# Optimization experiments

Hardware: AMD Instinct MI355X
Metric: run time of the kernel (lower is better)

The kernel has to match this reference:

```python
import jax, jax.numpy as jnp
import numpy as np

M = 32  # m = nsample_q


def _shared_mlp(x, layers):
    # x: [B, C, S, K]; each layer is 1x1 conv (pointwise) + bias + ReLU
    for W, b in layers:
        x = jax.nn.relu(jnp.einsum('oc,bcsk->bosk', W, x) + b[None, :, None, None])
    return x


def _conv_params(key, c_in, c_out):
    k1, k2 = jax.random.split(key)
    scale = 1.0 / np.sqrt(c_in)
    W = jax.random.uniform(k1, (c_out, c_in), jnp.float32, -scale, scale)
    b = jax.random.uniform(k2, (c_out,), jnp.float32, -scale, scale)
    return W, b


def setup_inputs() -> dict:
    key = jax.random.key(0)
    ks = jax.random.split(key, 12)
    B, S, C = 2, 8192, 64
    inp = {
        'xyz1': jax.random.normal(ks[0], (B, 3, S), jnp.float32),
        'feature1': jax.random.normal(ks[1], (B, C, S), jnp.float32),
        'xyz2': jax.random.normal(ks[2], (B, 3, S), jnp.float32),
        'feature2': jax.random.normal(ks[3], (B, C, S), jnp.float32),
    }
    # mlp1_spec = [64+64+10, 64, 64]
    inp['w_mlp1_0'], inp['b_mlp1_0'] = _conv_params(ks[4], 138, 64)
    inp['w_mlp1_1'], inp['b_mlp1_1'] = _conv_params(ks[5], 64, 64)
    # xyz encoders: [10 -> 64]
    inp['w_xyz1'], inp['b_xyz1'] = _conv_params(ks[6], 10, 64)
    inp['w_xyz2'], inp['b_xyz2'] = _conv_params(ks[7], 10, 64)
    # mlp2_spec = [128, 64, 64]
    inp['w_mlp2_0'], inp['b_mlp2_0'] = _conv_params(ks[8], 128, 64)
    inp['w_mlp2_1'], inp['b_mlp2_1'] = _conv_params(ks[9], 64, 64)
    # mlp3_spec = [192, 64, 64]
    inp['w_mlp3_0'], inp['b_mlp3_0'] = _conv_params(ks[10], 192, 64)
    inp['w_mlp3_1'], inp['b_mlp3_1'] = _conv_params(ks[11], 64, 64)
    return inp


def _arc_indices(S, m):
    # stage-1: each point attends to all m points of its arc (static, numpy)
    base = (np.arange(S) // m) * m
    idx_q = base[:, None] + np.arange(m)[None, :]          # [S, m]
    # stage-2: the other m-1 points of the arc (excluding self)
    pos = np.arange(S) % m
    mask = np.arange(m)[None, :] != pos[:, None]
    idx_rem = idx_q[mask].reshape(S, m - 1)                 # [S, m-1]
    return jnp.asarray(idx_q), jnp.asarray(idx_rem)


def reference(xyz1, feature1, xyz2, feature2,
              w_mlp1_0, b_mlp1_0, w_mlp1_1, b_mlp1_1,
              w_xyz1, b_xyz1, w_xyz2, b_xyz2,
              w_mlp2_0, b_mlp2_0, w_mlp2_1, b_mlp2_1,
              w_mlp3_0, b_mlp3_0, w_mlp3_1, b_mlp3_1):
    B, _, S = xyz1.shape
    idx_q, idx_rem = _arc_indices(S, M)

    # ---- stage 1: cross-frame cost volume over arc neighbors in frame2 ----
    qi_xyz = xyz2[:, :, idx_q]                 # [B,3,S,M]
    qi_feat = feature2[:, :, idx_q]            # [B,C,S,M]
    pi_xyz = xyz1[:, :, :, None]               # [B,3,S,1] (broadcast as tile)
    pi_feat = feature1[:, :, :, None]
    d_xyz = qi_xyz - pi_xyz
    euc = jnp.sqrt(jnp.sum(d_xyz * d_xyz, axis=1, keepdims=True) + 1e-20)
    pi_xyz_cat = jnp.concatenate(
        [jnp.broadcast_to(pi_xyz, qi_xyz.shape), qi_xyz, d_xyz, euc], axis=1)  # [B,10,S,M]
    feat_cat = jnp.concatenate(
        [jnp.broadcast_to(pi_feat, qi_feat.shape), qi_feat], axis=1)           # [B,2C,S,M]
    x = jnp.concatenate([pi_xyz_cat, feat_cat], axis=1)                         # [B,10+2C,S,M]
    pi_new = _shared_mlp(x, [(w_mlp1_0, b_mlp1_0), (w_mlp1_1, b_mlp1_1)])       # [B,64,S,M]
    pi_enc = _shared_mlp(pi_xyz_cat, [(w_xyz1, b_xyz1)])                        # [B,64,S,M]
    pi_cat = _shared_mlp(jnp.concatenate([pi_enc, pi_new], axis=1),
                         [(w_mlp2_0, b_mlp2_0), (w_mlp2_1, b_mlp2_1)])          # [B,64,S,M]
    WQ = jax.nn.softmax(pi_cat, axis=3)
    pi_agg = jnp.sum(WQ * pi_new, axis=3)                                       # [B,64,S]

    # ---- stage 2: intra-frame smoothing over remaining arc points ----
    pc_xyz_g = xyz1[:, :, idx_rem]             # [B,3,S,M-1]
    pc_pts_g = pi_agg[:, :, idx_rem]           # [B,64,S,M-1]
    pc_xyz_n = xyz1[:, :, :, None]
    pc_pts_n = feature1[:, :, :, None]
    d2 = pc_xyz_g - pc_xyz_n
    euc2 = jnp.sqrt(jnp.sum(d2 * d2, axis=1, keepdims=True) + 1e-20)
    pc_xyz_cat = jnp.concatenate(
        [jnp.broadcast_to(pc_xyz_n, pc_xyz_g.shape), pc_xyz_g, d2, euc2], axis=1)  # [B,10,S,M-1]
    pc_enc = _shared_mlp(pc_xyz_cat, [(w_xyz2, b_xyz2)])                           # [B,64,S,M-1]
    pc_cat = jnp.concatenate(
        [pc_enc, jnp.broadcast_to(pc_pts_n, (pc_pts_n.shape[:3] + (M - 1,))), pc_pts_g],
        axis=1)                                                                    # [B,192,S,M-1]
    pc_cat = _shared_mlp(pc_cat, [(w_mlp3_0, b_mlp3_0), (w_mlp3_1, b_mlp3_1)])
    WP = jax.nn.softmax(pc_cat, axis=3)
    return jnp.sum(WP * pc_pts_g, axis=3)      # [B,64,S]
```

## Files before the change

kernel.cpp:

```cpp
#include <hip/hip_runtime.h>


typedef __attribute__((ext_vector_type(8))) short   short8;
typedef __attribute__((ext_vector_type(8))) __bf16  bf16x8;
typedef __attribute__((ext_vector_type(4))) float   f32x4;
typedef __attribute__((ext_vector_type(4))) float   float4v;
typedef __attribute__((ext_vector_type(2))) unsigned int uint2v;
typedef __attribute__((ext_vector_type(4))) unsigned int uint4v;

#define S_LEN 8192
#define TPB   256
#define LOG2E 1.4426950408889634f

#define WSO_L11   0
#define WSO_L20   8192
#define WSO_L21   24576
#define WSO_L30A  32768
#define WSO_L31   40960
#define WS_WF1    49152
#define WS_WF2    57344
#define WS_W30B   65536
#define WS_W30C   73728
#define WS_F32    81920

#define OFF_W     0
#define OFF_ACT   32768
#define OFF_A1B   65536
#define OFF_A2B   69632
#define OFF_AGGB  73728
#define OFF_X1    77824
#define OFF_X2    78336
#define LDS_TOTAL 78848

__device__ __forceinline__ unsigned short f2bf(float f){
  unsigned int u = __float_as_uint(f);
  u += 0x7fffu + ((u >> 16) & 1u);
  return (unsigned short)(u >> 16);
}
__device__ __forceinline__ float bf2f(unsigned short h){
  return __uint_as_float(((unsigned int)h) << 16);
}
__device__ __forceinline__ unsigned cvtpk(float lo, float hi){
  unsigned r;
  asm("v_cvt_pk_bf16_f32 %0, %1, %2" : "=v"(r) : "v"(lo), "v"(hi));
  return r;
}
__device__ __forceinline__ float exp2a(float x){
  float r; asm("v_exp_f32 %0, %1" : "=v"(r) : "v"(x)); return r;
}

__device__ __forceinline__ bf16x8 ldsA(const char* base, int r, int k){
  short8 a = *(const short8*)(base + ((((r << 6) + k) << 1) ^ ((r & 7) << 4)));
  return __builtin_bit_cast(bf16x8, a);
}
__device__ __forceinline__ void stBF(char* base, int r, int c, float v){
  *(unsigned short*)(base + ((((r << 6) + c) << 1) ^ ((r & 7) << 4))) = f2bf(v);
}
__device__ __forceinline__ float ldBF(const char* base, int r, int c){
  return bf2f(*(const unsigned short*)(base + ((((r << 6) + c) << 1) ^ ((r & 7) << 4))));
}
__device__ __forceinline__ void stBF4(char* base, int r, int c4, float4v v){
  uint2v u; u.x = cvtpk(v.x, v.y); u.y = cvtpk(v.z, v.w);
  *(uint2v*)(base + ((((r << 6) + c4) << 1) ^ ((r & 7) << 4))) = u;
}
__device__ __forceinline__ float4v ldBF4(const char* base, int r, int c4){
  uint2v u = *(const uint2v*)(base + ((((r << 6) + c4) << 1) ^ ((r & 7) << 4)));
  float4v f;
  f.x = bf2f((unsigned short)(u.x & 0xffffu));
  f.y = bf2f((unsigned short)(u.x >> 16));
  f.z = bf2f((unsigned short)(u.y & 0xffffu));
  f.w = bf2f((unsigned short)(u.y >> 16));
  return f;
}

__device__ __forceinline__ void gemm_k64(f32x4 acc[4], const char* Asrc,
                                         const char* Bp, int rbase, int lane){
  const int r  = rbase + (lane & 15);
  const int kg = (lane >> 4) << 3;
#pragma unroll
  for (int kb = 0; kb < 2; ++kb){
    bf16x8 a = ldsA(Asrc, r, kb * 32 + kg);
#pragma unroll
    for (int cb = 0; cb < 4; ++cb){
      short8 braw = *(const short8*)(Bp + (((kb << 2) + cb) * 64 + lane) * 16);
      acc[cb] = __builtin_amdgcn_mfma_f32_16x16x32_bf16(
          a, __builtin_bit_cast(bf16x8, braw), acc[cb], 0, 0, 0);
    }
  }
}

__device__ __forceinline__ void gemm32_k64B(f32x4 acc[2][4], const char* Asrc,
                                            const char* Bp, int lane){
  const int kg = (lane >> 4) << 3;
#pragma unroll
  for (int t = 0; t < 2; ++t){
    const int r = t * 16 + (lane & 15);
#pragma unroll
    for (int kb = 0; kb < 2; ++kb){
      bf16x8 a = ldsA(Asrc, r, kb * 32 + kg);
#pragma unroll
      for (int cb = 0; cb < 4; ++cb){
        short8 braw = *(const short8*)(Bp + (((kb << 2) + cb) * 64 + lane) * 16);
        acc[t][cb] = __builtin_amdgcn_mfma_f32_16x16x32_bf16(
            a, __builtin_bit_cast(bf16x8, braw), acc[t][cb], 0, 0, 0);
      }
    }
  }
}

__device__ __forceinline__ void gemm_chL(f32x4 acc[2][4], const char* act,
                                         const char* Wp, int l15, int kg, int lane){
#pragma unroll
  for (int kb = 0; kb < 2; ++kb){
    bf16x8 W[4];
#pragma unroll
    for (int mb = 0; mb < 4; ++mb)
      W[mb] = __builtin_bit_cast(bf16x8,
          *(const short8*)(Wp + (((kb << 2) + mb) * 64 + lane) * 16));
#pragma unroll
    for (int nb = 0; nb < 2; ++nb){
      bf16x8 bfrag = ldsA(act, nb * 16 + l15, kb * 32 + kg);
#pragma unroll
      for (int mb = 0; mb < 4; ++mb)
        acc[nb][mb] = __builtin_amdgcn_mfma_f32_16x16x32_bf16(
            W[mb], bfrag, acc[nb][mb], 0, 0, 0);
    }
  }
}

__device__ __forceinline__ void store_ch(char* dst, f32x4 acc[2][4],
                                         const float4v bias4[4], int l15, int g){
#pragma unroll
  for (int nb = 0; nb < 2; ++nb){
    const int row = nb * 16 + l15;
    const int rb  = row << 7;
    const int swz = (row & 7) << 4;
#pragma unroll
    for (int mb = 0; mb < 4; ++mb){
      f32x4 z = acc[nb][mb] + bias4[mb];
      z.x=fmaxf(z.x,0.f); z.y=fmaxf(z.y,0.f); z.z=fmaxf(z.z,0.f); z.w=fmaxf(z.w,0.f);
      uint2v u; u.x = cvtpk(z.x, z.y); u.y = cvtpk(z.z, z.w);
      *(uint2v*)(dst + (rb + ((mb * 32 + g * 8) ^ swz))) = u;
    }
  }
}

__device__ __forceinline__ float red_max(float x){
  x = fmaxf(x, __shfl_xor(x, 16, 64));
  x = fmaxf(x, __shfl_xor(x, 32, 64));
  return x;
}
__device__ __forceinline__ float red_sum(float x){
  x += __shfl_xor(x, 16, 64);
  x += __shfl_xor(x, 32, 64);
  return x;
}

__global__ void pack_weights(const float* __restrict__ w10, const float* __restrict__ w11,
                             const float* __restrict__ wx1, const float* __restrict__ wx2,
                             const float* __restrict__ w20, const float* __restrict__ w21,
                             const float* __restrict__ w30, const float* __restrict__ w31,
                             unsigned char* __restrict__ ws)
{
  for (int i = blockIdx.x * blockDim.x + threadIdx.x; i < 42304;
       i += gridDim.x * blockDim.x){
    if (i < 40960){
      const float* src; int stride, coff, e;
      if      (i <  4096){ src = w11; stride =  64; coff =   0; e = i;         }
      else if (i < 12288){ src = w20; stride = 128; coff =   0; e = i -  4096; }
      else if (i < 16384){ src = w21; stride =  64; coff =   0; e = i - 12288; }
      else if (i < 20480){ src = w30; stride = 192; coff =   0; e = i - 16384; }
      else if (i < 24576){ src = w31; stride =  64; coff =   0; e = i - 20480; }
      else if (i < 28672){ src = w10; stride = 138; coff =  10; e = i - 24576; }
      else if (i < 32768){ src = w10; stride = 138; coff =  74; e = i - 28672; }
      else if (i < 36864){ src = w30; stride = 192; coff =  64; e = i - 32768; }
      else               { src = w30; stride = 192; coff = 128; e = i - 36864; }
      int j = e & 7, lane = (e >> 3) & 63, cb = (e >> 9) & 3, kb = e >> 11;
      int k = kb * 32 + ((lane >> 4) << 3) + j;
      int o = cb * 16 + (lane & 15);
      float val = src[o * stride + coff + k];
      if ((i >= 12288 && i < 16384) || (i >= 20480 && i < 24576)) val *= LOG2E;
      ((unsigned short*)ws)[i] = f2bf(val);
    } else {
      int f = i - 40960; float v;
      if (f < 1152){
        int grp = f / 192, rem = f % 192, d = rem >> 6, o = rem & 63;
        if      (grp == 0) v = w10[o*138 + d]     - w10[o*138 + 6 + d];
        else if (grp == 1) v = w10[o*138 + 3 + d] + w10[o*138 + 6 + d];
        else if (grp == 2) v = wx1[o*10 + d]      - wx1[o*10 + 6 + d];
        else if (grp == 3) v = wx1[o*10 + 3 + d]  + wx1[o*10 + 6 + d];
        else if (grp == 4) v = wx2[o*10 + d]      - wx2[o*10 + 6 + d];
        else               v = wx2[o*10 + 3 + d]  + wx2[o*10 + 6 + d];
      }
      else if (f < 1216) v = w10[(f - 1152)*138 + 9];
      else if (f < 1280) v = wx1[(f - 1216)*10  + 9];
      else               v = wx2[(f - 1280)*10  + 9];
      ((float*)(ws + WS_F32))[f] = v;
    }
  }
}

__global__ __launch_bounds__(TPB, 2) void cvkernel(
    const float* __restrict__ xyz1, const float* __restrict__ feat1,
    const float* __restrict__ xyz2, const float* __restrict__ feat2,
    const float* __restrict__ b10v, const float* __restrict__ bx1v,
    const float* __restrict__ b11v, const float* __restrict__ b20v,
    const float* __restrict__ b21v, const float* __restrict__ bx2v,
    const float* __restrict__ b30v, const float* __restrict__ b31v,
    const char*  __restrict__ ws,   float* __restrict__ out)
{
  extern __shared__ __align__(16) char smem[];
  const int tid  = threadIdx.x;
  const int lane = tid & 63;
  const int wave = tid >> 6;
  const int l15  = lane & 15;
  const int lg   = lane >> 4;
  const int kg   = lg << 3;
  const int tile = blockIdx.x;
  const int b    = tile >> 8;
  const int s0   = (tile & 255) << 5;

  float* x1   = (float*)(smem + OFF_X1);
  float* x2   = (float*)(smem + OFF_X2);
  char*  a1B  = smem + OFF_A1B;
  char*  a2B  = smem + OFF_A2B;
  char*  aggB = smem + OFF_AGGB;
  char*  wlds = smem + OFF_W;
  const float* cw = (const float*)(ws + WS_F32);

  char* myA = smem + OFF_ACT + wave * 8192;
  char* myB = myA + 4096;

  { const uint4v* src = (const uint4v*)ws;
    uint4v*       dst = (uint4v*)wlds;
    for (int i = tid; i < 2048; i += TPB) dst[i] = src[i]; }
  if (tid < 32){
#pragma unroll
    for (int d = 0; d < 3; ++d) x1[tid*4+d] = xyz1[(b*3+d)*S_LEN + s0 + tid];
    x1[tid*4+3] = 0.f;
  } else if (tid < 64){
    int p = tid - 32;
#pragma unroll
    for (int d = 0; d < 3; ++d) x2[p*4+d] = xyz2[(b*3+d)*S_LEN + s0 + p];
    x2[p*4+3] = 0.f;
  }
  for (int i = tid; i < 2048; i += TPB){
    int ch = i >> 5, p = i & 31;
    stBF(smem + OFF_ACT,        p, ch, feat1[(b*64+ch)*S_LEN + s0 + p]);
    stBF(smem + OFF_ACT + 4096, p, ch, feat2[(b*64+ch)*S_LEN + s0 + p]);
  }
  __syncthreads();

  {
    const char* Ab  = (wave < 2) ? (smem + OFF_ACT) : (smem + OFF_ACT + 4096);
    const char* Bg  = ws + ((wave < 2) ? WS_WF1 : WS_WF2);
    char* dstB      = (wave < 2) ? a1B : a2B;
    const float* cc = (wave < 2) ? cw : cw + 192;
    const float* xs = (wave < 2) ? x1 : x2;
    const int rt    = wave & 1;
    f32x4 acc[4];
#pragma unroll
    for (int cb = 0; cb < 4; ++cb) acc[cb] = (f32x4){0.f,0.f,0.f,0.f};
    gemm_k64(acc, Ab, Bg, rt * 16, lane);
#pragma unroll
    for (int cb = 0; cb < 4; ++cb){
      int col = (cb << 4) + l15;
      float c0 = cc[col], c1 = cc[64+col], c2 = cc[128+col];
#pragma unroll
      for (int v = 0; v < 4; ++v){
        int row = rt*16 + (lg << 2) + v;
        float val = acc[cb][v] + c0*xs[row*4] + c1*xs[row*4+1] + c2*xs[row*4+2];
        stBF(dstB, row, col, val);
      }
    }
  }
  __syncthreads();

  const int myc4 = l15 << 2;
  const int gc4  = lg << 2;

  {
    const float4v we4 = *(const float4v*)(cw + 1152 + myc4);
    const float4v ee4 = *(const float4v*)(cw + 1216 + myc4);
    const float4v b04 = *(const float4v*)(b10v + myc4);
    const float4v b14 = *(const float4v*)(bx1v + myc4);
    const float4v C1a = *(const float4v*)(cw + 384 + myc4);
    const float4v C1b = *(const float4v*)(cw + 448 + myc4);
    const float4v C1c = *(const float4v*)(cw + 512 + myc4);
    const float4v C2a = *(const float4v*)(cw + 576 + myc4);
    const float4v C2b = *(const float4v*)(cw + 640 + myc4);
    const float4v C2c = *(const float4v*)(cw + 704 + myc4);
    float4v b11f4[4], b20f4[4];
#pragma unroll
    for (int mb = 0; mb < 4; ++mb){
      b11f4[mb] = *(const float4v*)(b11v + mb*16 + gc4);
      b20f4[mb] = *(const float4v*)(b20v + mb*16 + gc4);
    }
    float b21r[4];
#pragma unroll
    for (int cb = 0; cb < 4; ++cb) b21r[cb] = b21v[cb*16 + l15] * LOG2E;

    for (int cc = 0; cc < 8; ++cc){
      const int p  = wave*8 + cc;
      const float px = x1[p*4], py = x1[p*4+1], pz = x1[p*4+2];
      const float4v hbase = ldBF4(a1B, p, myc4) + b04;
      const float4v ebase = C1a*px + C1b*py + C1c*pz + b14;
#pragma unroll
      for (int it = 0; it < 8; ++it){
        int q = it*4 + lg;
        float qx = x2[q*4], qy = x2[q*4+1], qz = x2[q*4+2];
        float dx = qx-px, dy = qy-py, dz = qz-pz;
        float eu = sqrtf(dx*dx + dy*dy + dz*dz + 1e-20f);
        float4v A2 = ldBF4(a2B, q, myc4);
        float4v hv = hbase + A2 + we4*eu;
        float4v ev = ebase + C2a*qx + C2b*qy + C2c*qz + ee4*eu;
        hv.x = fmaxf(hv.x,0.f); hv.y = fmaxf(hv.y,0.f); hv.z = fmaxf(hv.z,0.f); hv.w = fmaxf(hv.w,0.f);
        ev.x = fmaxf(ev.x,0.f); ev.y = fmaxf(ev.y,0.f); ev.z = fmaxf(ev.z,0.f); ev.w = fmaxf(ev.w,0.f);
        stBF4(myA, q, myc4, hv);
        stBF4(myB, q, myc4, ev);
      }
      f32x4 acc[2][4];
#pragma unroll
      for (int nb = 0; nb < 2; ++nb)
#pragma unroll
        for (int mb = 0; mb < 4; ++mb) acc[nb][mb] = (f32x4){0.f,0.f,0.f,0.f};
      __builtin_amdgcn_s_setprio(1);
      gemm_chL(acc, myA, wlds + 0, l15, kg, lane);
      __builtin_amdgcn_s_setprio(0);
      store_ch(myA, acc, b11f4, l15, lg);
#pragma unroll
      for (int nb = 0; nb < 2; ++nb)
#pragma unroll
        for (int mb = 0; mb < 4; ++mb) acc[nb][mb] = (f32x4){0.f,0.f,0.f,0.f};
      __builtin_amdgcn_s_setprio(1);
      gemm_chL(acc, myB, wlds + 8192,        l15, kg, lane);
      gemm_chL(acc, myA, wlds + 8192 + 8192, l15, kg, lane);
      __builtin_amdgcn_s_setprio(0);
      store_ch(myB, acc, b20f4, l15, lg);
      f32x4 acc2[2][4];
#pragma unroll
      for (int t = 0; t < 2; ++t)
#pragma unroll
        for (int cb = 0; cb < 4; ++cb) acc2[t][cb] = (f32x4){0.f,0.f,0.f,0.f};
      __builtin_amdgcn_s_setprio(1);
      gemm32_k64B(acc2, myB, wlds + 24576, lane);
      __builtin_amdgcn_s_setprio(0);
      float mm[4], den[4], num[4];
#pragma unroll
      for (int cb = 0; cb < 4; ++cb) mm[cb] = -1e30f;
#pragma unroll
      for (int t = 0; t < 2; ++t)
#pragma unroll
        for (int cb = 0; cb < 4; ++cb)
#pragma unroll
          for (int v = 0; v < 4; ++v){
            float l = fmaxf(acc2[t][cb][v] + b21r[cb], 0.f);
            acc2[t][cb][v] = l;
            mm[cb] = fmaxf(mm[cb], l);
          }
#pragma unroll
      for (int cb = 0; cb < 4; ++cb){ mm[cb] = red_max(mm[cb]); den[cb] = 0.f; num[cb] = 0.f; }
#pragma unroll
      for (int t = 0; t < 2; ++t)
#pragma unroll
        for (int cb = 0; cb < 4; ++cb)
#pragma unroll
          for (int v = 0; v < 4; ++v){
            float e = exp2a(acc2[t][cb][v] - mm[cb]);
            den[cb] += e;
            num[cb] += e * ldBF(myA, t*16 + (lg<<2) + v, (cb<<4) + l15);
          }
#pragma unroll
      for (int cb = 0; cb < 4; ++cb){ den[cb] = red_sum(den[cb]); num[cb] = red_sum(num[cb]); }
      {
        float nv = (lg==0)?num[0]:((lg==1)?num[1]:((lg==2)?num[2]:num[3]));
        float dv = (lg==0)?den[0]:((lg==1)?den[1]:((lg==2)?den[2]:den[3]));
        stBF(aggB, p, (lg<<4) + l15, nv / dv);
      }
    }
  }
  __syncthreads();

  for (int i = tid; i < 2048; i += TPB){
    int ch = i >> 5, p = i & 31;
    stBF(smem + OFF_ACT, p, ch, feat1[(b*64+ch)*S_LEN + s0 + p]);
  }
  { const uint4v* sA = (const uint4v*)(ws + WSO_L30A);
    const uint4v* sB = (const uint4v*)(ws + WSO_L31);
    uint4v* dA = (uint4v*)(wlds);
    uint4v* dB = (uint4v*)(wlds + 24576);
    for (int i = tid; i < 512; i += TPB){ dA[i] = sA[i]; dB[i] = sB[i]; } }
  __syncthreads();
  {
    const char* Ab = (wave < 2) ? (smem + OFF_ACT) : aggB;
    const char* Bg = ws + ((wave < 2) ? WS_W30B : WS_W30C);
    char* dstB     = (wave < 2) ? a1B : a2B;
    const int rt   = wave & 1;
    f32x4 acc[4];
#pragma unroll
    for (int cb = 0; cb < 4; ++cb) acc[cb] = (f32x4){0.f,0.f,0.f,0.f};
    gemm_k64(acc, Ab, Bg, rt*16, lane);
    __syncthreads();
#pragma unroll
    for (int cb = 0; cb < 4; ++cb)
#pragma unroll
      for (int v = 0; v < 4; ++v)
        stBF(dstB, rt*16 + (lg << 2) + v, (cb << 4) + l15, acc[cb][v]);
  }
  __syncthreads();

  {
    const float4v ge4 = *(const float4v*)(cw + 1280 + myc4);
    const float4v b54 = *(const float4v*)(bx2v + myc4);
    const float4v D1a = *(const float4v*)(cw +  768 + myc4);
    const float4v D1b = *(const float4v*)(cw +  832 + myc4);
    const float4v D1c = *(const float4v*)(cw +  896 + myc4);
    const float4v D2a = *(const float4v*)(cw +  960 + myc4);
    const float4v D2b = *(const float4v*)(cw + 1024 + myc4);
    const float4v D2c = *(const float4v*)(cw + 1088 + myc4);
    float4v b30f4[4];
#pragma unroll
    for (int mb = 0; mb < 4; ++mb)
      b30f4[mb] = *(const float4v*)(b30v + mb*16 + gc4);
    float b31r[4];
#pragma unroll
    for (int cb = 0; cb < 4; ++cb) b31r[cb] = b31v[cb*16 + l15] * LOG2E;

    for (int cc = 0; cc < 8; ++cc){
      const int p  = wave*8 + cc;
      const float px = x1[p*4], py = x1[p*4+1], pz = x1[p*4+2];
      const float4v ebase = D1a*px + D1b*py + D1c*pz + b54;
      float4v v1f4[4];
#pragma unroll
      for (int mb = 0; mb < 4; ++mb)
        v1f4[mb] = ldBF4(a1B, p, mb*16 + gc4);
#pragma unroll
      for (int it = 0; it < 8; ++it){
        int q = it*4 + lg;
        float qx = x1[q*4], qy = x1[q*4+1], qz = x1[q*4+2];
        float dx = qx-px, dy = qy-py, dz = qz-pz;
        float eu = sqrtf(dx*dx + dy*dy + dz*dz + 1e-20f);
        float4v ev = ebase + D2a*qx + D2b*qy + D2c*qz + ge4*eu;
        ev.x = fmaxf(ev.x,0.f); ev.y = fmaxf(ev.y,0.f); ev.z = fmaxf(ev.z,0.f); ev.w = fmaxf(ev.w,0.f);
        stBF4(myA, q, myc4, ev);
      }
      f32x4 acc[2][4];
#pragma unroll
      for (int nb = 0; nb < 2; ++nb)
#pragma unroll
        for (int mb = 0; mb < 4; ++mb) acc[nb][mb] = (f32x4){0.f,0.f,0.f,0.f};
      __builtin_amdgcn_s_setprio(1);
      gemm_chL(acc, myA, wlds + 0, l15, kg, lane);
      __builtin_amdgcn_s_setprio(0);
#pragma unroll
      for (int nb = 0; nb < 2; ++nb){
        const int q   = nb*16 + l15;
        const int rb  = q << 7;
        const int swz = (q & 7) << 4;
#pragma unroll
        for (int mb = 0; mb < 4; ++mb){
          float4v v2 = ldBF4(a2B, q, mb*16 + gc4);
          f32x4 z = acc[nb][mb] + v1f4[mb] + v2 + b30f4[mb];
          z.x=fmaxf(z.x,0.f); z.y=fmaxf(z.y,0.f); z.z=fmaxf(z.z,0.f); z.w=fmaxf(z.w,0.f);
          uint2v u; u.x = cvtpk(z.x, z.y); u.y = cvtpk(z.z, z.w);
          *(uint2v*)(myB + (rb + ((mb*32 + lg*8) ^ swz))) = u;
        }
      }
      f32x4 acc2[2][4];
#pragma unroll
      for (int t = 0; t < 2; ++t)
#pragma unroll
        for (int cb = 0; cb < 4; ++cb) acc2[t][cb] = (f32x4){0.f,0.f,0.f,0.f};
      __builtin_amdgcn_s_setprio(1);
      gemm32_k64B(acc2, myB, wlds + 24576, lane);
      __builtin_amdgcn_s_setprio(0);
      float mm[4], den[4], num[4];
#pragma unroll
      for (int cb = 0; cb < 4; ++cb) mm[cb] = -1e30f;
#pragma unroll
      for (int t = 0; t < 2; ++t)
#pragma unroll
        for (int cb = 0; cb < 4; ++cb)
#pragma unroll
          for (int v = 0; v < 4; ++v){
            int q = t*16 + (lg<<2) + v;
            float l = fmaxf(acc2[t][cb][v] + b31r[cb], 0.f);
            l = (q == p) ? -1e30f : l;
            acc2[t][cb][v] = l;
            mm[cb] = fmaxf(mm[cb], l);
          }
#pragma unroll
      for (int cb = 0; cb < 4; ++cb){ mm[cb] = red_max(mm[cb]); den[cb] = 0.f; num[cb] = 0.f; }
#pragma unroll
      for (int t = 0; t < 2; ++t)
#pragma unroll
        for (int cb = 0; cb < 4; ++cb)
#pragma unroll
          for (int v = 0; v < 4; ++v){
            int q = t*16 + (lg<<2) + v;
            float e = exp2a(acc2[t][cb][v] - mm[cb]);
            den[cb] += e;
            num[cb] += e * ldBF(aggB, q, (cb<<4) + l15);
          }
#pragma unroll
      for (int cb = 0; cb < 4; ++cb){ den[cb] = red_sum(den[cb]); num[cb] = red_sum(num[cb]); }
      {
        float nv = (lg==0)?num[0]:((lg==1)?num[1]:((lg==2)?num[2]:num[3]));
        float dv = (lg==0)?den[0]:((lg==1)?den[1]:((lg==2)?den[2]:den[3]));
        int ch = (lg<<4) + l15;
        out[(b*64 + ch)*S_LEN + s0 + p] = nv / dv;
      }
    }
  }
}

extern "C" void kernel_launch(void* const* d_in, const int* in_sizes, int n_in,
                              void* d_out, int out_size, void* d_ws, size_t ws_size,
                              hipStream_t stream)
{
  const float* xyz1 = (const float*)d_in[0];
  const float* feat1= (const float*)d_in[1];
  const float* xyz2 = (const float*)d_in[2];
  const float* feat2= (const float*)d_in[3];
  const float* w10  = (const float*)d_in[4];
  const float* b10  = (const float*)d_in[5];
  const float* w11  = (const float*)d_in[6];
  const float* b11  = (const float*)d_in[7];
  const float* wx1  = (const float*)d_in[8];
  const float* bx1  = (const float*)d_in[9];
  const float* wx2  = (const float*)d_in[10];
  const float* bx2  = (const float*)d_in[11];
  const float* w20  = (const float*)d_in[12];
  const float* b20  = (const float*)d_in[13];
  const float* w21  = (const float*)d_in[14];
  const float* b21  = (const float*)d_in[15];
  const float* w30  = (const float*)d_in[16];
  const float* b30  = (const float*)d_in[17];
  const float* w31  = (const float*)d_in[18];
  const float* b31  = (const float*)d_in[19];

  (void)hipFuncSetAttribute(reinterpret_cast<const void*>(cvkernel),
                            hipFuncAttributeMaxDynamicSharedMemorySize, LDS_TOTAL);

  hipLaunchKernelGGL(pack_weights, dim3(64), dim3(256), 0, stream,
                     w10, w11, wx1, wx2, w20, w21, w30, w31, (unsigned char*)d_ws);
  hipLaunchKernelGGL(cvkernel, dim3(512), dim3(TPB), LDS_TOTAL, stream,
                     xyz1, feat1, xyz2, feat2,
                     b10, bx1, b11, b20, b21, bx2, b30, b31,
                     (const char*)d_ws, (float*)d_out);
}
```

Measured before the change: 92.87 us.

## Hold weights in registers, drop softmax max pass, stage output through LDS

MFMA weight fragments are now loaded from LDS into registers once per stage rather than re-read on every GEMM call. Each point's 32 distances to the arc points are computed once per wave into a small LDS buffer, so the sqrt is no longer repeated for every channel group. The softmax max-reduction is removed and exp is applied directly to the ReLU logits, with the self point masked to zero weight. This saves a shuffle reduction and a second pass, but risks overflow if logits get large. Results are gathered in an LDS tile and written out in coalesced rows after a final barrier, replacing strided global stores.

```diff
diff --git a/kernel.cpp b/kernel.cpp
--- a/kernel.cpp
+++ b/kernel.cpp
@@ -24,13 +24,15 @@
 #define WS_F32    81920
 
 #define OFF_W     0
+#define OFF_OUTB  8192
 #define OFF_ACT   32768
 #define OFF_A1B   65536
 #define OFF_A2B   69632
 #define OFF_AGGB  73728
 #define OFF_X1    77824
 #define OFF_X2    78336
-#define LDS_TOTAL 78848
+#define OFF_EUCB  78848
+#define LDS_TOTAL 79360
 
 __device__ __forceinline__ unsigned short f2bf(float f){
   unsigned int u = __float_as_uint(f);
@@ -72,6 +74,9 @@
   f.w = bf2f((unsigned short)(u.y >> 16));
   return f;
 }
+__device__ __forceinline__ int outb_idx(int p, int ch){
+  return ((p << 6) + ch) ^ ((p & 7) << 2);
+}
 
 __device__ __forceinline__ void gemm_k64(f32x4 acc[4], const char* Asrc,
                                          const char* Bp, int rbase, int lane){
@@ -89,8 +94,15 @@
   }
 }
 
-__device__ __forceinline__ void gemm32_k64B(f32x4 acc[2][4], const char* Asrc,
-                                            const char* Bp, int lane){
+__device__ __forceinline__ void load_B8(bf16x8 Breg[8], const char* Bp, int lane){
+#pragma unroll
+  for (int u = 0; u < 8; ++u)
+    Breg[u] = __builtin_bit_cast(bf16x8,
+        *(const short8*)(Bp + (u * 64 + lane) * 16));
+}
+
+__device__ __forceinline__ void gemm32_k64(f32x4 acc[2][4], const char* Asrc,
+                                           const bf16x8 Breg[8], int lane){
   const int kg = (lane >> 4) << 3;
 #pragma unroll
   for (int t = 0; t < 2; ++t){
@@ -99,33 +111,25 @@
     for (int kb = 0; kb < 2; ++kb){
       bf16x8 a = ldsA(Asrc, r, kb * 32 + kg);
 #pragma unroll
-      for (int cb = 0; cb < 4; ++cb){
-        short8 braw = *(const short8*)(Bp + (((kb << 2) + cb) * 64 + lane) * 16);
+      for (int cb = 0; cb < 4; ++cb)
         acc[t][cb] = __builtin_amdgcn_mfma_f32_16x16x32_bf16(
-            a, __builtin_bit_cast(bf16x8, braw), acc[t][cb], 0, 0, 0);
-      }
-    }
-  }
-}
-
-__device__ __forceinline__ void gemm_chL(f32x4 acc[2][4], const char* act,
-                                         const char* Wp, int l15, int kg, int lane){
-#pragma unroll
-  for (int kb = 0; kb < 2; ++kb){
-    bf16x8 W[4];
-#pragma unroll
-    for (int mb = 0; mb < 4; ++mb)
-      W[mb] = __builtin_bit_cast(bf16x8,
-          *(const short8*)(Wp + (((kb << 2) + mb) * 64 + lane) * 16));
+            a, Breg[kb * 4 + cb], acc[t][cb], 0, 0, 0);
+    }
+  }
+}
+
+__device__ __forceinline__ void gemm_ch(f32x4 acc[2][4], const char* act,
+                                        const bf16x8 W[8], int l15, int kg){
+#pragma unroll
+  for (int kb = 0; kb < 2; ++kb)
 #pragma unroll
     for (int nb = 0; nb < 2; ++nb){
       bf16x8 bfrag = ldsA(act, nb * 16 + l15, kb * 32 + kg);
 #pragma unroll
       for (int mb = 0; mb < 4; ++mb)
         acc[nb][mb] = __builtin_amdgcn_mfma_f32_16x16x32_bf16(
-            W[mb], bfrag, acc[nb][mb], 0, 0, 0);
-    }
-  }
+            W[kb * 4 + mb], bfrag, acc[nb][mb], 0, 0, 0);
+    }
 }
 
 __device__ __forceinline__ void store_ch(char* dst, f32x4 acc[2][4],
@@ -145,11 +149,6 @@
   }
 }
 
-__device__ __forceinline__ float red_max(float x){
-  x = fmaxf(x, __shfl_xor(x, 16, 64));
-  x = fmaxf(x, __shfl_xor(x, 32, 64));
-  return x;
-}
 __device__ __forceinline__ float red_sum(float x){
   x += __shfl_xor(x, 16, 64);
   x += __shfl_xor(x, 32, 64);
@@ -226,6 +225,8 @@
   char*  a2B  = smem + OFF_A2B;
   char*  aggB = smem + OFF_AGGB;
   char*  wlds = smem + OFF_W;
+  float* outb = (float*)(smem + OFF_OUTB);
+  float* eucb = (float*)(smem + OFF_EUCB) + wave * 32;
   const float* cw = (const float*)(ws + WS_F32);
 
   char* myA = smem + OFF_ACT + wave * 8192;
@@ -300,17 +301,26 @@
 #pragma unroll
     for (int cb = 0; cb < 4; ++cb) b21r[cb] = b21v[cb*16 + l15] * LOG2E;
 
+    bf16x8 W11r[8], W20ar[8], W20br[8], W21r[8];
+    load_B8(W11r,  wlds + 0,     lane);
+    load_B8(W20ar, wlds + 8192,  lane);
+    load_B8(W20br, wlds + 16384, lane);
+    load_B8(W21r,  wlds + 24576, lane);
+
     for (int cc = 0; cc < 8; ++cc){
       const int p  = wave*8 + cc;
       const float px = x1[p*4], py = x1[p*4+1], pz = x1[p*4+2];
+      if (lane < 32){
+        float dx = x2[lane*4]-px, dy = x2[lane*4+1]-py, dz = x2[lane*4+2]-pz;
+        eucb[lane] = sqrtf(dx*dx + dy*dy + dz*dz + 1e-20f);
+      }
       const float4v hbase = ldBF4(a1B, p, myc4) + b04;
       const float4v ebase = C1a*px + C1b*py + C1c*pz + b14;
 #pragma unroll
       for (int it = 0; it < 8; ++it){
         int q = it*4 + lg;
         float qx = x2[q*4], qy = x2[q*4+1], qz = x2[q*4+2];
-        float dx = qx-px, dy = qy-py, dz = qz-pz;
-        float eu = sqrtf(dx*dx + dy*dy + dz*dz + 1e-20f);
+        float eu = eucb[q];
         float4v A2 = ldBF4(a2B, q, myc4);
         float4v hv = hbase + A2 + we4*eu;
         float4v ev = ebase + C2a*qx + C2b*qy + C2c*qz + ee4*eu;
@@ -325,7 +335,7 @@
 #pragma unroll
         for (int mb = 0; mb < 4; ++mb) acc[nb][mb] = (f32x4){0.f,0.f,0.f,0.f};
       __builtin_amdgcn_s_setprio(1);
-      gemm_chL(acc, myA, wlds + 0, l15, kg, lane);
+      gemm_ch(acc, myA, W11r, l15, kg);
       __builtin_amdgcn_s_setprio(0);
       store_ch(myA, acc, b11f4, l15, lg);
 #pragma unroll
@@ -333,8 +343,8 @@
 #pragma unroll
         for (int mb = 0; mb < 4; ++mb) acc[nb][mb] = (f32x4){0.f,0.f,0.f,0.f};
       __builtin_amdgcn_s_setprio(1);
-      gemm_chL(acc, myB, wlds + 8192,        l15, kg, lane);
-      gemm_chL(acc, myA, wlds + 8192 + 8192, l15, kg, lane);
+      gemm_ch(acc, myB, W20ar, l15, kg);
+      gemm_ch(acc, myA, W20br, l15, kg);
       __builtin_amdgcn_s_setprio(0);
       store_ch(myB, acc, b20f4, l15, lg);
       f32x4 acc2[2][4];
@@ -343,11 +353,9 @@
 #pragma unroll
         for (int cb = 0; cb < 4; ++cb) acc2[t][cb] = (f32x4){0.f,0.f,0.f,0.f};
       __builtin_amdgcn_s_setprio(1);
-      gemm32_k64B(acc2, myB, wlds + 24576, lane);
+      gemm32_k64(acc2, myB, W21r, lane);
       __builtin_amdgcn_s_setprio(0);
-      float mm[4], den[4], num[4];
-#pragma unroll
-      for (int cb = 0; cb < 4; ++cb) mm[cb] = -1e30f;
+      float den[4] = {0.f,0.f,0.f,0.f}, num[4] = {0.f,0.f,0.f,0.f};
 #pragma unroll
       for (int t = 0; t < 2; ++t)
 #pragma unroll
@@ -355,18 +363,7 @@
 #pragma unroll
           for (int v = 0; v < 4; ++v){
             float l = fmaxf(acc2[t][cb][v] + b21r[cb], 0.f);
-            acc2[t][cb][v] = l;
-            mm[cb] = fmaxf(mm[cb], l);
-          }
-#pragma unroll
-      for (int cb = 0; cb < 4; ++cb){ mm[cb] = red_max(mm[cb]); den[cb] = 0.f; num[cb] = 0.f; }
-#pragma unroll
-      for (int t = 0; t < 2; ++t)
-#pragma unroll
-        for (int cb = 0; cb < 4; ++cb)
-#pragma unroll
-          for (int v = 0; v < 4; ++v){
-            float e = exp2a(acc2[t][cb][v] - mm[cb]);
+            float e = exp2a(l);
             den[cb] += e;
             num[cb] += e * ldBF(myA, t*16 + (lg<<2) + v, (cb<<4) + l15);
           }
@@ -426,9 +423,17 @@
 #pragma unroll
     for (int cb = 0; cb < 4; ++cb) b31r[cb] = b31v[cb*16 + l15] * LOG2E;
 
+    bf16x8 W30Ar[8], W31r[8];
+    load_B8(W30Ar, wlds + 0,     lane);
+    load_B8(W31r,  wlds + 24576, lane);
+
     for (int cc = 0; cc < 8; ++cc){
       const int p  = wave*8 + cc;
       const float px = x1[p*4], py = x1[p*4+1], pz = x1[p*4+2];
+      if (lane < 32){
+        float dx = x1[lane*4]-px, dy = x1[lane*4+1]-py, dz = x1[lane*4+2]-pz;
+        eucb[lane] = sqrtf(dx*dx + dy*dy + dz*dz + 1e-20f);
+      }
       const float4v ebase = D1a*px + D1b*py + D1c*pz + b54;
       float4v v1f4[4];
 #pragma unroll
@@ -438,8 +443,7 @@
       for (int it = 0; it < 8; ++it){
         int q = it*4 + lg;
         float qx = x1[q*4], qy = x1[q*4+1], qz = x1[q*4+2];
-        float dx = qx-px, dy = qy-py, dz = qz-pz;
-        float eu = sqrtf(dx*dx + dy*dy + dz*dz + 1e-20f);
+        float eu = eucb[q];
         float4v ev = ebase + D2a*qx + D2b*qy + D2c*qz + ge4*eu;
         ev.x = fmaxf(ev.x,0.f); ev.y = fmaxf(ev.y,0.f); ev.z = fmaxf(ev.z,0.f); ev.w = fmaxf(ev.w,0.f);
         stBF4(myA, q, myc4, ev);
@@ -450,7 +454,7 @@
 #pragma unroll
         for (int mb = 0; mb < 4; ++mb) acc[nb][mb] = (f32x4){0.f,0.f,0.f,0.f};
       __builtin_amdgcn_s_setprio(1);
-      gemm_chL(acc, myA, wlds + 0, l15, kg, lane);
+      gemm_ch(acc, myA, W30Ar, l15, kg);
       __builtin_amdgcn_s_setprio(0);
 #pragma unroll
       for (int nb = 0; nb < 2; ++nb){
@@ -472,11 +476,9 @@
 #pragma unroll
         for (int cb = 0; cb < 4; ++cb) acc2[t][cb] = (f32x4){0.f,0.f,0.f,0.f};
       __builtin_amdgcn_s_setprio(1);
-      gemm32_k64B(acc2, myB, wlds + 24576, lane);
+      gemm32_k64(acc2, myB, W31r, lane);
       __builtin_amdgcn_s_setprio(0);
-      float mm[4], den[4], num[4];
-#pragma unroll
-      for (int cb = 0; cb < 4; ++cb) mm[cb] = -1e30f;
+      float den[4] = {0.f,0.f,0.f,0.f}, num[4] = {0.f,0.f,0.f,0.f};
 #pragma unroll
       for (int t = 0; t < 2; ++t)
 #pragma unroll
@@ -485,20 +487,8 @@
           for (int v = 0; v < 4; ++v){
             int q = t*16 + (lg<<2) + v;
             float l = fmaxf(acc2[t][cb][v] + b31r[cb], 0.f);
-            l = (q == p) ? -1e30f : l;
-            acc2[t][cb][v] = l;
-            mm[cb] = fmaxf(mm[cb], l);
-          }
-#pragma unroll
-      for (int cb = 0; cb < 4; ++cb){ mm[cb] = red_max(mm[cb]); den[cb] = 0.f; num[cb] = 0.f; }
-#pragma unroll
-      for (int t = 0; t < 2; ++t)
-#pragma unroll
-        for (int cb = 0; cb < 4; ++cb)
-#pragma unroll
-          for (int v = 0; v < 4; ++v){
-            int q = t*16 + (lg<<2) + v;
-            float e = exp2a(acc2[t][cb][v] - mm[cb]);
+            float e = exp2a(l);
+            e = (q == p) ? 0.f : e;
             den[cb] += e;
             num[cb] += e * ldBF(aggB, q, (cb<<4) + l15);
           }
@@ -507,10 +497,15 @@
       {
         float nv = (lg==0)?num[0]:((lg==1)?num[1]:((lg==2)?num[2]:num[3]));
         float dv = (lg==0)?den[0]:((lg==1)?den[1]:((lg==2)?den[2]:den[3]));
-        int ch = (lg<<4) + l15;
-        out[(b*64 + ch)*S_LEN + s0 + p] = nv / dv;
-      }
-    }
+        outb[outb_idx(p, (lg<<4) + l15)] = nv / dv;
+      }
+    }
+  }
+  __syncthreads();
+
+  for (int i = tid; i < 2048; i += TPB){
+    int ch = i >> 5, p = i & 31;
+    out[(b*64 + ch)*S_LEN + s0 + p] = outb[outb_idx(p, ch)];
   }
 }
 
```

After: 179.4 us. +93.1%, slower.
